# Optimization experiments

Measured on AMD Instinct MI355X. Metric: run time of the kernel, lower is better.

The kernel has to match this reference:

```python
import jax, jax.numpy as jnp
import numpy as np

B, N, C = 4, 4096, 1024
H, D = 16, 64
EPS = 1e-6


def setup_inputs() -> dict:
    key = jax.random.key(0)
    ks = jax.random.split(key, 7)
    x = jax.random.normal(ks[0], (B, N, C), dtype=jnp.float32)
    # True = PAD (PyTorch convention)
    src_key_padding_mask = jax.random.randint(ks[1], (B, N), 0, 2).astype(jnp.bool_)
    s = 1.0 / np.sqrt(C)
    W_qkv = jax.random.uniform(ks[2], (3 * C, C), jnp.float32, -s, s)
    b_qkv = jax.random.uniform(ks[3], (3 * C,), jnp.float32, -s, s)
    W_out = jax.random.uniform(ks[4], (C, C), jnp.float32, -s, s)
    b_out = jax.random.uniform(ks[5], (C,), jnp.float32, -s, s)
    return {"x": x, "W_qkv": W_qkv, "b_qkv": b_qkv, "W_out": W_out,
            "b_out": b_out, "src_key_padding_mask": src_key_padding_mask}


def _phi(t):
    # elu(t) + 1  (alpha=1)
    return jnp.where(t > 0, t + 1.0, jnp.exp(t))


def reference(x, W_qkv, b_qkv, W_out, b_out, src_key_padding_mask):
    # qkv projection: [B,N,3C] -> [3,B,H,N,D]
    qkv = (x @ W_qkv.T + b_qkv).reshape(B, N, 3, H, D).transpose(2, 0, 3, 1, 4)
    q, k, v = qkv[0], qkv[1], qkv[2]
    qf = _phi(q)
    kf = _phi(k)
    valid = (~src_key_padding_mask).astype(kf.dtype)[:, None, :, None]  # [B,1,N,1]
    kf = kf * valid
    v = v * valid
    # kv state: [B,H,D,D]; z: [B,H,D]
    kv = jnp.einsum('bhnd,bhne->bhde', kf, v)
    z = kf.sum(axis=2)
    y_num = jnp.einsum('bhnd,bhde->bhne', qf, kv)      # [B,H,N,D]
    y_den = jnp.einsum('bhnd,bhd->bhn', qf, z)          # [B,H,N]
    y_den = jnp.maximum(y_den, EPS)[..., None]
    y = (y_num / y_den).transpose(0, 2, 1, 3).reshape(B, N, C)
    return y @ W_out.T + b_out
```

## Files before the change

kernel.cpp:

```cpp
#include <hip/hip_runtime.h>
#include <math.h>

#define B_ 4
#define N_ 4096
#define C_ 1024
#define H_ 16
#define D_ 64
#define M_ (B_*N_)
#define GK 1024
#define NCH 8
#define CHROWS (N_/NCH)

typedef __attribute__((ext_vector_type(8))) _Float16 f16x8;
typedef __attribute__((ext_vector_type(4))) _Float16 f16x4;
typedef __attribute__((ext_vector_type(4))) float f32x4;

__device__ __forceinline__ float phi_f(float t) {
  return (t > 0.0f) ? (t + 1.0f) : __expf(t);
}

#define GLOAD(gp, lp) __builtin_amdgcn_global_load_lds( \
    (const __attribute__((address_space(1))) unsigned int*)(gp), \
    (__attribute__((address_space(3))) unsigned int*)(lp), 16, 0, 0)

#define BARM() asm volatile("s_barrier" ::: "memory")
#define WAITV6() asm volatile("s_waitcnt vmcnt(6)" ::: "memory")
#define WAITV4() asm volatile("s_waitcnt vmcnt(4)" ::: "memory")
#define WAITV0() asm volatile("s_waitcnt vmcnt(0)" ::: "memory")
#define PRIO1() __builtin_amdgcn_s_setprio(1)
#define PRIO0() __builtin_amdgcn_s_setprio(0)

__device__ __forceinline__ f32x4 mfma16h(f16x8 a, f16x8 b, f32x4 c) {
  return __builtin_amdgcn_mfma_f32_16x16x32_f16(a, b, c, 0, 0, 0);
}

__global__ __launch_bounds__(256) void prep_k(
    const float* __restrict__ x, _Float16* __restrict__ Xh,
    const float* __restrict__ Wq, _Float16* __restrict__ Wqh, _Float16* __restrict__ Wql,
    const float* __restrict__ Wo, _Float16* __restrict__ Woh, _Float16* __restrict__ Wol,
    const void* __restrict__ mask, float* __restrict__ valid) {
  const int b = blockIdx.x, tid = threadIdx.x;
  if (b < 16384) {
    int i = b * 256 + tid;
    float4 v = ((const float4*)x)[i];
    f16x4 h;
    h[0] = (_Float16)v.x; h[1] = (_Float16)v.y;
    h[2] = (_Float16)v.z; h[3] = (_Float16)v.w;
    ((f16x4*)Xh)[i] = h;
  } else if (b < 19456) {
    int i = (b - 16384) * 256 + tid;
    float4 v = ((const float4*)Wq)[i];
    float vs[4] = {v.x, v.y, v.z, v.w};
    f16x4 hv, lv;
#pragma unroll
    for (int q = 0; q < 4; ++q) {
      _Float16 hh = (_Float16)vs[q];
      lv[q] = (_Float16)(vs[q] - (float)hh);
      hv[q] = hh;
    }
    ((f16x4*)Wqh)[i] = hv;
    ((f16x4*)Wql)[i] = lv;
  } else if (b < 20480) {
    int i = (b - 19456) * 256 + tid;
    float4 v = ((const float4*)Wo)[i];
    float vs[4] = {v.x, v.y, v.z, v.w};
    f16x4 hv, lv;
#pragma unroll
    for (int q = 0; q < 4; ++q) {
      _Float16 hh = (_Float16)vs[q];
      lv[q] = (_Float16)(vs[q] - (float)hh);
      hv[q] = hh;
    }
    ((f16x4*)Woh)[i] = hv;
    ((f16x4*)Wol)[i] = lv;
  } else {
    __shared__ unsigned int sni, snf;
    if (tid == 0) { sni = 0u; snf = 0u; }
    __syncthreads();
    const unsigned int* mw = (const unsigned int*)mask;
    unsigned int ni = 0, nf = 0;
    for (int t = tid; t < 4096; t += 256) {
      unsigned int v = mw[t];
      ni |= (v > 1u) ? 1u : 0u;
      nf |= (v != 0u && v != 0x3F800000u) ? 1u : 0u;
    }
    if (ni) atomicOr(&sni, 1u);
    if (nf) atomicOr(&snf, 1u);
    __syncthreads();
    const int f = (!sni) ? 0 : ((!snf) ? 1 : 2);
    int i = (b - 20480) * 256 + tid;
    int m;
    if (f == 0)      m = ((const int*)mask)[i] != 0;
    else if (f == 1) m = ((const float*)mask)[i] != 0.0f;
    else             m = ((const unsigned char*)mask)[i] != 0;
    valid[i] = m ? 0.0f : 1.0f;
  }
}


#define TILE_BODY(PC, DO_STAGE, DO_PRE, WAITK, KS)                             \
  {                                                                            \
    const _Float16* bb = lds + (PC) * 24576;                                   \
    const _Float16* nb = lds + (((PC) + 1) % 3) * 24576;                       \
    _Float16* sq = lds + (((PC) + 2) % 3) * 24576;                             \
    const size_t ks = (KS);                                                    \
                                     \
    _Pragma("unroll") for (int j = 0; j < 4; ++j)                              \
      bl[j] = *(const f16x8*)&bb[16384 + (wj * 4 + j) * 512 + lane * 8];       \
    if (DO_STAGE) { GLOAD(A + gA0 + ks, sq + w * 512);                         \
                    GLOAD(A + gA1 + ks, sq + 4096 + w * 512); }                \
    BARM();                                                                    \
    PRIO1();                                                                   \
    _Pragma("unroll") for (int i = 0; i < 4; ++i)                              \
      _Pragma("unroll") for (int j = 0; j < 4; ++j)                            \
        acc[i][j] = mfma16h(a0[i], bh[j], acc[i][j]);                          \
    PRIO0();                                                                   \
        \
    _Pragma("unroll") for (int i = 0; i < 4; ++i)                              \
      a1[i] = *(const f16x8*)&bb[(wm * 8 + 4 + i) * 512 + lane * 8];           \
    if (DO_STAGE) { GLOAD(Bh + gB0 + ks, sq + 8192 + w * 512);                 \
                    GLOAD(Bh + gB1 + ks, sq + 12288 + w * 512); }              \
    if ((WAITK) == 1) { WAITV4(); } else if ((WAITK) == 2) { WAITV0(); }       \
    BARM();                                                                    \
    PRIO1();                                                                   \
    _Pragma("unroll") for (int i = 0; i < 4; ++i)                              \
      _Pragma("unroll") for (int j = 0; j < 4; ++j)                            \
        acc[i][j] = mfma16h(a0[i], bl[j], acc[i][j]);                          \
    PRIO0();                                                                   \
                                \
    if (DO_PRE) { _Pragma("unroll") for (int i = 0; i < 4; ++i)                \
      a0[i] = *(const f16x8*)&nb[(wm * 8 + i) * 512 + lane * 8]; }             \
    if (DO_STAGE) { GLOAD(Bl + gB0 + ks, sq + 16384 + w * 512);                \
                    GLOAD(Bl + gB1 + ks, sq + 20480 + w * 512); }              \
    BARM();                                                                    \
    PRIO1();                                                                   \
    _Pragma("unroll") for (int i = 0; i < 4; ++i)                              \
      _Pragma("unroll") for (int j = 0; j < 4; ++j)                            \
        acc[4 + i][j] = mfma16h(a1[i], bh[j], acc[4 + i][j]);                  \
    PRIO0();                                                                   \
                                          \
    if (DO_PRE) { _Pragma("unroll") for (int j = 0; j < 4; ++j)                \
      bh[j] = *(const f16x8*)&nb[8192 + (wj * 4 + j) * 512 + lane * 8]; }      \
    BARM();                                                                    \
    PRIO1();                                                                   \
    _Pragma("unroll") for (int i = 0; i < 4; ++i)                              \
      _Pragma("unroll") for (int j = 0; j < 4; ++j)                            \
        acc[4 + i][j] = mfma16h(a1[i], bl[j], acc[4 + i][j]);                  \
    PRIO0();                                                                   \
  }

template <int EPI>
__global__ __launch_bounds__(512, 2) void gemm256_k(
    const _Float16* __restrict__ A,
    const _Float16* __restrict__ Bh, const _Float16* __restrict__ Bl,
    const float* __restrict__ bias, const float* __restrict__ valid,
    float* __restrict__ qf, float* __restrict__ kf, float* __restrict__ vv,
    float* __restrict__ outp, int jb) {
  __shared__ _Float16 lds[73728];
  const int tid = threadIdx.x;
  const int lane = tid & 63, w = tid >> 6;
  const int lm = lane & 15, lq = lane >> 4;
  const int wm = w >> 2, wj = w & 3;

  const int nwg = gridDim.x;
  const int q8 = nwg >> 3;
  const int wid = (blockIdx.x & 7) * q8 + (blockIdx.x >> 3);
  const int j_blk = wid >> 6;
  const int m_blk = wid & 63;
  const int m0 = m_blk * 256;
  const int jg0 = jb + j_blk * 256;

  const size_t gA0 = (size_t)(m0 + w * 16 + lm) * GK + lq * 8;
  const size_t gA1 = gA0 + (size_t)128 * GK;
  const size_t gB0 = (size_t)(jg0 + w * 16 + lm) * GK + lq * 8;
  const size_t gB1 = gB0 + (size_t)128 * GK;

#pragma unroll
  for (int tt = 0; tt < 2; ++tt) {
    _Float16* sq = lds + tt * 24576;
    const size_t ks = (size_t)tt * 32;
    GLOAD(A + gA0 + ks, sq + w * 512);
    GLOAD(A + gA1 + ks, sq + 4096 + w * 512);
    GLOAD(Bh + gB0 + ks, sq + 8192 + w * 512);
    GLOAD(Bh + gB1 + ks, sq + 12288 + w * 512);
    GLOAD(Bl + gB0 + ks, sq + 16384 + w * 512);
    GLOAD(Bl + gB1 + ks, sq + 20480 + w * 512);
  }
  WAITV6();
  BARM();

  f32x4 acc[8][4] = {};
  f16x8 a0[4], a1[4], bh[4], bl[4];
#pragma unroll
  for (int i = 0; i < 4; ++i)
    a0[i] = *(const f16x8*)&lds[(wm * 8 + i) * 512 + lane * 8];
#pragma unroll
  for (int j = 0; j < 4; ++j)
    bh[j] = *(const f16x8*)&lds[8192 + (wj * 4 + j) * 512 + lane * 8];

  for (int it = 0; it < 10; ++it) {
    const int t0 = 3 * it;
    TILE_BODY(0, true, true, 1, (size_t)(t0 + 2) * 32)
    TILE_BODY(1, true, true, 1, (size_t)(t0 + 3) * 32)
    TILE_BODY(2, true, true, 1, (size_t)(t0 + 4) * 32)
  }
  TILE_BODY(0, false, true, 2, 0)
  TILE_BODY(1, false, false, 0, 0)

  if (EPI == 0) {
    const int ty = jg0 >> 10;
    float* dst = (ty == 0) ? qf : ((ty == 1) ? kf : vv);
    float vld[8][4];
#pragma unroll
    for (int i = 0; i < 8; ++i)
#pragma unroll
      for (int r = 0; r < 4; ++r)
        vld[i][r] = (ty == 0) ? 1.0f : valid[m0 + wm * 128 + i * 16 + lq * 4 + r];
#pragma unroll
    for (int jt = 0; jt < 4; ++jt) {
      int jcol = jg0 + wj * 64 + jt * 16 + lm;
      float bj = bias[jcol];
      int c = jcol & 1023, hd = c >> 6, d = c & 63;
#pragma unroll
      for (int i = 0; i < 8; ++i)
#pragma unroll
        for (int r = 0; r < 4; ++r) {
          int m = m0 + wm * 128 + i * 16 + lq * 4 + r;
          int b = m >> 12, n = m & 4095;
          float val = acc[i][jt][r] + bj;
          if (ty <= 1) val = phi_f(val);
          if (ty >= 1) val *= vld[i][r];
          dst[(((size_t)(b * H_ + hd) * N_ + n) << 6) + d] = val;
        }
    }
  } else {
#pragma unroll
    for (int jt = 0; jt < 4; ++jt) {
      int jcol = jg0 + wj * 64 + jt * 16 + lm;
      float bj = bias[jcol];
#pragma unroll
      for (int i = 0; i < 8; ++i)
#pragma unroll
        for (int r = 0; r < 4; ++r) {
          int m = m0 + wm * 128 + i * 16 + lq * 4 + r;
          outp[(size_t)m * C_ + jcol] = acc[i][jt][r] + bj;
        }
    }
  }
}

__global__ __launch_bounds__(256) void kv_partial_k(
    const float* __restrict__ kf, const float* __restrict__ vv,
    float* __restrict__ kvp, float* __restrict__ zp) {
  const int bh = blockIdx.x, ch = blockIdx.y;
  const float* kfr = kf + ((size_t)bh * N_ + ch * CHROWS) * 64;
  const float* vr  = vv + ((size_t)bh * N_ + ch * CHROWS) * 64;
  __shared__ float vs[16][64];
  const int tid = threadIdx.x;
  const int d4 = tid >> 4, e4 = tid & 15;
  const int srow = tid >> 4, scol = (tid & 15) * 4;
  float acc[4][4] = {};
  float zacc[4] = {};
  for (int nb = 0; nb < CHROWS; nb += 16) {
    float4 st = *(const float4*)&vr[(size_t)(nb + srow) * 64 + scol];
    __syncthreads();
    *(float4*)&vs[srow][scol] = st;
    float4 kq[16];
#pragma unroll
    for (int r = 0; r < 16; ++r)
      kq[r] = *(const float4*)&kfr[(size_t)(nb + r) * 64 + d4 * 4];
    __syncthreads();
#pragma unroll
    for (int r = 0; r < 16; ++r) {
      float4 vq = *(const float4*)&vs[r][e4 * 4];
      float kk[4] = {kq[r].x, kq[r].y, kq[r].z, kq[r].w};
      float vk[4] = {vq.x, vq.y, vq.z, vq.w};
#pragma unroll
      for (int di = 0; di < 4; ++di) {
        if (e4 == 0) zacc[di] += kk[di];
#pragma unroll
        for (int ei = 0; ei < 4; ++ei) acc[di][ei] += kk[di] * vk[ei];
      }
    }
  }
  size_t base = ((size_t)bh * NCH + ch) * 4096 + (size_t)d4 * 4 * 64 + e4 * 4;
#pragma unroll
  for (int di = 0; di < 4; ++di)
    *(float4*)&kvp[base + (size_t)di * 64] =
        make_float4(acc[di][0], acc[di][1], acc[di][2], acc[di][3]);
  if (e4 == 0)
    *(float4*)&zp[((size_t)bh * NCH + ch) * 64 + d4 * 4] =
        make_float4(zacc[0], zacc[1], zacc[2], zacc[3]);
}

__global__ __launch_bounds__(256) void kv_reduce_k(
    const float* __restrict__ kvp, const float* __restrict__ zp,
    float* __restrict__ kv, float* __restrict__ z) {
  const int bh = blockIdx.x, tid = threadIdx.x;
  for (int i = tid; i < 4096; i += 256) {
    float s = 0.f;
#pragma unroll
    for (int c = 0; c < NCH; ++c) s += kvp[((size_t)bh * NCH + c) * 4096 + i];
    kv[(size_t)bh * 4096 + i] = s;
  }
  if (tid < 64) {
    float s = 0.f;
#pragma unroll
    for (int c = 0; c < NCH; ++c) s += zp[((size_t)bh * NCH + c) * 64 + tid];
    z[bh * 64 + tid] = s;
  }
}

__global__ __launch_bounds__(256) void attn_apply_k(
    const float* __restrict__ qf, const float* __restrict__ kv,
    const float* __restrict__ z, _Float16* __restrict__ Y) {
  const int bh = blockIdx.x, nt = blockIdx.y;
  const int b = bh >> 4, hd = bh & 15;
  __shared__ float qs[128][65];
  __shared__ float kvs[64][68];
  __shared__ float zs[64];
  __shared__ float dens[128];
  const int tid = threadIdx.x;
  const float* qrow = qf + ((size_t)bh * N_ + nt * 128) * 64;
#pragma unroll
  for (int i = 0; i < 4; ++i) {
    int fl = tid + i * 256;
    int d = fl >> 4, cc = (fl & 15) * 4;
    float4 t4 = *(const float4*)&kv[(size_t)bh * 4096 + d * 64 + cc];
    kvs[d][cc] = t4.x; kvs[d][cc+1] = t4.y; kvs[d][cc+2] = t4.z; kvs[d][cc+3] = t4.w;
  }
  if (tid < 64) zs[tid] = z[bh * 64 + tid];
#pragma unroll
  for (int i = 0; i < 8; ++i) {
    int fl = tid + i * 256;
    int r = fl >> 4, cc = (fl & 15) * 4;
    float4 t4 = *(const float4*)&qrow[(size_t)r * 64 + cc];
    qs[r][cc] = t4.x; qs[r][cc+1] = t4.y; qs[r][cc+2] = t4.z; qs[r][cc+3] = t4.w;
  }
  __syncthreads();
  {
    int n = tid >> 1, half = tid & 1;
    float s = 0.f;
#pragma unroll
    for (int dd = 0; dd < 32; ++dd) {
      int d = half * 32 + dd;
      s += qs[n][d] * zs[d];
    }
    float other = __shfl_down(s, 1);
    if (half == 0) dens[n] = fmaxf(s + other, 1e-6f);
  }
  __syncthreads();
  const int ng = tid >> 3, eg = tid & 7;
  float acc[4][8] = {};
  for (int d = 0; d < 64; ++d) {
    float kvrow[8];
    *(float4*)&kvrow[0] = *(const float4*)&kvs[d][eg * 8];
    *(float4*)&kvrow[4] = *(const float4*)&kvs[d][eg * 8 + 4];
#pragma unroll
    for (int i = 0; i < 4; ++i) {
      float a = qs[ng * 4 + i][d];
#pragma unroll
      for (int j = 0; j < 8; ++j) acc[i][j] += a * kvrow[j];
    }
  }
#pragma unroll
  for (int i = 0; i < 4; ++i) {
    int nl = ng * 4 + i;
    int n = nt * 128 + nl;
    float inv = 1.0f / dens[nl];
    size_t off = ((size_t)b * N_ + n) * C_ + hd * 64 + eg * 8;
    f16x8 hv;
#pragma unroll
    for (int j = 0; j < 8; ++j) hv[j] = (_Float16)(acc[i][j] * inv);
    *(f16x8*)&Y[off] = hv;
  }
}

extern "C" void kernel_launch(void* const* d_in, const int* in_sizes, int n_in,
                              void* d_out, int out_size, void* d_ws, size_t ws_size,
                              hipStream_t stream) {
  const float* x      = (const float*)d_in[0];
  const float* W_qkv  = (const float*)d_in[1];
  const float* b_qkv  = (const float*)d_in[2];
  const float* W_out  = (const float*)d_in[3];
  const float* b_out  = (const float*)d_in[4];
  const void*  mask   = d_in[5];
  float* out = (float*)d_out;

  const size_t bhnd = (size_t)B_ * H_ * N_ * D_;
  float* ws = (float*)d_ws;
  float* buf1 = ws;
  float* buf2 = ws + bhnd;
  _Float16* Xh  = (_Float16*)(ws + 2 * bhnd);
  _Float16* Wqh = Xh + bhnd;
  _Float16* Wql = Wqh + (size_t)3072 * 1024;
  _Float16* Woh = Wql + (size_t)3072 * 1024;
  _Float16* Wol = Woh + (size_t)1024 * 1024;
  float* tail2 = (float*)(Wol + (size_t)1024 * 1024);
  float* kvp = tail2;
  float* zp  = kvp + (size_t)64 * NCH * 4096;
  float* kv  = zp + (size_t)64 * NCH * 64;
  float* z   = kv + (size_t)64 * 4096;
  float* valid = z + 64 * 64;

  _Float16* Y = (_Float16*)buf2;

  prep_k<<<20544, 256, 0, stream>>>(x, Xh, W_qkv, Wqh, Wql, W_out, Woh, Wol,
                                    mask, valid);
  gemm256_k<0><<<512, 512, 0, stream>>>(
      Xh, Wqh, Wql, b_qkv, valid, buf1, buf1, buf2, nullptr, 1024);
  kv_partial_k<<<dim3(B_ * H_, NCH), 256, 0, stream>>>(buf1, buf2, kvp, zp);
  kv_reduce_k<<<B_ * H_, 256, 0, stream>>>(kvp, zp, kv, z);
  gemm256_k<0><<<256, 512, 0, stream>>>(
      Xh, Wqh, Wql, b_qkv, valid, buf1, buf1, buf2, nullptr, 0);
  attn_apply_k<<<dim3(B_ * H_, N_ / 128), 256, 0, stream>>>(buf1, kv, z, Y);
  gemm256_k<1><<<256, 512, 0, stream>>>(
      Y, Woh, Wol, b_out, valid, nullptr, nullptr, nullptr, out, 0);
}
```

Before: 483.8 us.

## Fuse attention apply into Q-projection GEMM epilogue using MFMA split-fp16

Result: no change. 475.7 us (-1.7%).

```diff
diff --git a/kernel.cpp b/kernel.cpp
--- a/kernel.cpp
+++ b/kernel.cpp
@@ -27,6 +27,8 @@
 #define WAITV6() asm volatile("s_waitcnt vmcnt(6)" ::: "memory")
 #define WAITV4() asm volatile("s_waitcnt vmcnt(4)" ::: "memory")
 #define WAITV0() asm volatile("s_waitcnt vmcnt(0)" ::: "memory")
+#define WAITL0() asm volatile("s_waitcnt lgkmcnt(0)" ::: "memory")
+#define SCHEDB() __builtin_amdgcn_sched_barrier(0)
 #define PRIO1() __builtin_amdgcn_s_setprio(1)
 #define PRIO0() __builtin_amdgcn_s_setprio(0)
 
@@ -155,7 +157,9 @@
     const _Float16* __restrict__ Bh, const _Float16* __restrict__ Bl,
     const float* __restrict__ bias, const float* __restrict__ valid,
     float* __restrict__ qf, float* __restrict__ kf, float* __restrict__ vv,
-    float* __restrict__ outp, int jb) {
+    float* __restrict__ outp, int jb, int jshift,
+    const _Float16* __restrict__ kvt_h, const _Float16* __restrict__ kvt_l,
+    const float* __restrict__ zv, _Float16* __restrict__ Yo) {
   __shared__ _Float16 lds[73728];
   const int tid = threadIdx.x;
   const int lane = tid & 63, w = tid >> 6;
@@ -165,8 +169,8 @@
   const int nwg = gridDim.x;
   const int q8 = nwg >> 3;
   const int wid = (blockIdx.x & 7) * q8 + (blockIdx.x >> 3);
-  const int j_blk = wid >> 6;
-  const int m_blk = wid & 63;
+  const int j_blk = wid & ((1 << jshift) - 1);
+  const int m_blk = wid >> jshift;
   const int m0 = m_blk * 256;
   const int jg0 = jb + j_blk * 256;
 
@@ -233,7 +237,7 @@
           dst[(((size_t)(b * H_ + hd) * N_ + n) << 6) + d] = val;
         }
     }
-  } else {
+  } else if (EPI == 1) {
 #pragma unroll
     for (int jt = 0; jt < 4; ++jt) {
       int jcol = jg0 + wj * 64 + jt * 16 + lm;
@@ -245,6 +249,92 @@
           int m = m0 + wm * 128 + i * 16 + lq * 4 + r;
           outp[(size_t)m * C_ + jcol] = acc[i][jt][r] + bj;
         }
+    }
+  } else {
+    const int head = (jg0 >> 6) + wj;
+    const int bidx = m0 >> 12;
+    const int bh_idx = bidx * H_ + head;
+    const size_t kvbase = (size_t)bh_idx * 4096;
+    float breg[4], zreg[4];
+#pragma unroll
+    for (int jt = 0; jt < 4; ++jt) {
+      breg[jt] = bias[jg0 + wj * 64 + jt * 16 + lm];
+      zreg[jt] = zv[bh_idx * 64 + jt * 16 + lm];
+    }
+    float den[8][4];
+#pragma unroll
+    for (int i = 0; i < 8; ++i)
+#pragma unroll
+      for (int r = 0; r < 4; ++r) {
+        float p = 0.f;
+#pragma unroll
+        for (int jt = 0; jt < 4; ++jt) {
+          float v = phi_f(acc[i][jt][r] + breg[jt]);
+          acc[i][jt][r] = v;
+          p += v * zreg[jt];
+        }
+        p += __shfl_xor(p, 1); p += __shfl_xor(p, 2);
+        p += __shfl_xor(p, 4); p += __shfl_xor(p, 8);
+        den[i][r] = 1.0f / fmaxf(p, 1e-6f);
+      }
+    BARM();
+    char* sb = (char*)(lds) + w * 16384;
+#pragma unroll
+    for (int h = 0; h < 2; ++h) {
+#pragma unroll
+      for (int i2 = 0; i2 < 4; ++i2) {
+#pragma unroll
+        for (int jt = 0; jt < 4; ++jt)
+#pragma unroll
+          for (int r = 0; r < 4; ++r) {
+            int row = i2 * 16 + lq * 4 + r;
+            int d = jt * 16 + lm;
+            float v = acc[h * 4 + i2][jt][r];
+            _Float16 vh = (_Float16)v;
+            _Float16 vl = (_Float16)(v - (float)vh);
+            int bo = (row * 128 + d * 2) ^ ((row & 7) << 4);
+            *(_Float16*)(sb + bo) = vh;
+            *(_Float16*)(sb + 8192 + bo) = vl;
+          }
+      }
+      WAITL0(); SCHEDB();
+      f32x4 acc2[4][4] = {};
+#pragma unroll
+      for (int ks = 0; ks < 2; ++ks) {
+        f16x8 ah[4], al[4], bhf[4], blf[4];
+#pragma unroll
+        for (int f = 0; f < 4; ++f) {
+          int row = f * 16 + lm;
+          int bo = (row * 128 + ks * 64 + lq * 16) ^ ((row & 7) << 4);
+          ah[f] = *(const f16x8*)(sb + bo);
+          al[f] = *(const f16x8*)(sb + 8192 + bo);
+        }
+#pragma unroll
+        for (int et = 0; et < 4; ++et) {
+          size_t go = kvbase + (size_t)(et * 16 + lm) * 64 + ks * 32 + lq * 8;
+          bhf[et] = *(const f16x8*)&kvt_h[go];
+          blf[et] = *(const f16x8*)&kvt_l[go];
+        }
+#pragma unroll
+        for (int f = 0; f < 4; ++f)
+#pragma unroll
+          for (int et = 0; et < 4; ++et) {
+            acc2[f][et] = mfma16h(ah[f], bhf[et], acc2[f][et]);
+            acc2[f][et] = mfma16h(ah[f], blf[et], acc2[f][et]);
+            acc2[f][et] = mfma16h(al[f], bhf[et], acc2[f][et]);
+          }
+      }
+#pragma unroll
+      for (int f = 0; f < 4; ++f)
+#pragma unroll
+        for (int et = 0; et < 4; ++et)
+#pragma unroll
+          for (int r = 0; r < 4; ++r) {
+            int m = m0 + wm * 128 + h * 64 + f * 16 + lq * 4 + r;
+            float yv = acc2[f][et][r] * den[h * 4 + f][r];
+            Yo[(size_t)m * C_ + head * 64 + et * 16 + lm] = (_Float16)yv;
+          }
+      WAITL0(); SCHEDB();
     }
   }
 }
@@ -295,84 +385,23 @@
 
 __global__ __launch_bounds__(256) void kv_reduce_k(
     const float* __restrict__ kvp, const float* __restrict__ zp,
-    float* __restrict__ kv, float* __restrict__ z) {
+    _Float16* __restrict__ kvt_h, _Float16* __restrict__ kvt_l,
+    float* __restrict__ z) {
   const int bh = blockIdx.x, tid = threadIdx.x;
   for (int i = tid; i < 4096; i += 256) {
     float s = 0.f;
 #pragma unroll
     for (int c = 0; c < NCH; ++c) s += kvp[((size_t)bh * NCH + c) * 4096 + i];
-    kv[(size_t)bh * 4096 + i] = s;
+    int d = i >> 6, e = i & 63;
+    _Float16 sh = (_Float16)s;
+    kvt_h[(size_t)bh * 4096 + e * 64 + d] = sh;
+    kvt_l[(size_t)bh * 4096 + e * 64 + d] = (_Float16)(s - (float)sh);
   }
   if (tid < 64) {
     float s = 0.f;
 #pragma unroll
     for (int c = 0; c < NCH; ++c) s += zp[((size_t)bh * NCH + c) * 64 + tid];
     z[bh * 64 + tid] = s;
-  }
-}
-
-__global__ __launch_bounds__(256) void attn_apply_k(
-    const float* __restrict__ qf, const float* __restrict__ kv,
-    const float* __restrict__ z, _Float16* __restrict__ Y) {
-  const int bh = blockIdx.x, nt = blockIdx.y;
-  const int b = bh >> 4, hd = bh & 15;
-  __shared__ float qs[128][65];
-  __shared__ float kvs[64][68];
-  __shared__ float zs[64];
-  __shared__ float dens[128];
-  const int tid = threadIdx.x;
-  const float* qrow = qf + ((size_t)bh * N_ + nt * 128) * 64;
-#pragma unroll
-  for (int i = 0; i < 4; ++i) {
-    int fl = tid + i * 256;
-    int d = fl >> 4, cc = (fl & 15) * 4;
-    float4 t4 = *(const float4*)&kv[(size_t)bh * 4096 + d * 64 + cc];
-    kvs[d][cc] = t4.x; kvs[d][cc+1] = t4.y; kvs[d][cc+2] = t4.z; kvs[d][cc+3] = t4.w;
-  }
-  if (tid < 64) zs[tid] = z[bh * 64 + tid];
-#pragma unroll
-  for (int i = 0; i < 8; ++i) {
-    int fl = tid + i * 256;
-    int r = fl >> 4, cc = (fl & 15) * 4;
-    float4 t4 = *(const float4*)&qrow[(size_t)r * 64 + cc];
-    qs[r][cc] = t4.x; qs[r][cc+1] = t4.y; qs[r][cc+2] = t4.z; qs[r][cc+3] = t4.w;
-  }
-  __syncthreads();
-  {
-    int n = tid >> 1, half = tid & 1;
-    float s = 0.f;
-#pragma unroll
-    for (int dd = 0; dd < 32; ++dd) {
-      int d = half * 32 + dd;
-      s += qs[n][d] * zs[d];
-    }
-    float other = __shfl_down(s, 1);
-    if (half == 0) dens[n] = fmaxf(s + other, 1e-6f);
-  }
-  __syncthreads();
-  const int ng = tid >> 3, eg = tid & 7;
-  float acc[4][8] = {};
-  for (int d = 0; d < 64; ++d) {
-    float kvrow[8];
-    *(float4*)&kvrow[0] = *(const float4*)&kvs[d][eg * 8];
-    *(float4*)&kvrow[4] = *(const float4*)&kvs[d][eg * 8 + 4];
-#pragma unroll
-    for (int i = 0; i < 4; ++i) {
-      float a = qs[ng * 4 + i][d];
-#pragma unroll
-      for (int j = 0; j < 8; ++j) acc[i][j] += a * kvrow[j];
-    }
-  }
-#pragma unroll
-  for (int i = 0; i < 4; ++i) {
-    int nl = ng * 4 + i;
-    int n = nt * 128 + nl;
-    float inv = 1.0f / dens[nl];
-    size_t off = ((size_t)b * N_ + n) * C_ + hd * 64 + eg * 8;
-    f16x8 hv;
-#pragma unroll
-    for (int j = 0; j < 8; ++j) hv[j] = (_Float16)(acc[i][j] * inv);
-    *(f16x8*)&Y[off] = hv;
   }
 }
 
@@ -399,21 +428,24 @@
   float* tail2 = (float*)(Wol + (size_t)1024 * 1024);
   float* kvp = tail2;
   float* zp  = kvp + (size_t)64 * NCH * 4096;
-  float* kv  = zp + (size_t)64 * NCH * 64;
-  float* z   = kv + (size_t)64 * 4096;
+  float* z   = zp + (size_t)64 * NCH * 64;
   float* valid = z + 64 * 64;
+  _Float16* kvt_h = (_Float16*)(valid + M_);
+  _Float16* kvt_l = kvt_h + (size_t)64 * 4096;
 
   _Float16* Y = (_Float16*)buf2;
 
   prep_k<<<20544, 256, 0, stream>>>(x, Xh, W_qkv, Wqh, Wql, W_out, Woh, Wol,
                                     mask, valid);
   gemm256_k<0><<<512, 512, 0, stream>>>(
-      Xh, Wqh, Wql, b_qkv, valid, buf1, buf1, buf2, nullptr, 1024);
+      Xh, Wqh, Wql, b_qkv, valid, buf1, buf1, buf2, nullptr, 1024, 3,
+      nullptr, nullptr, nullptr, nullptr);
   kv_partial_k<<<dim3(B_ * H_, NCH), 256, 0, stream>>>(buf1, buf2, kvp, zp);
-  kv_reduce_k<<<B_ * H_, 256, 0, stream>>>(kvp, zp, kv, z);
-  gemm256_k<0><<<256, 512, 0, stream>>>(
-      Xh, Wqh, Wql, b_qkv, valid, buf1, buf1, buf2, nullptr, 0);
-  attn_apply_k<<<dim3(B_ * H_, N_ / 128), 256, 0, stream>>>(buf1, kv, z, Y);
+  kv_reduce_k<<<B_ * H_, 256, 0, stream>>>(kvp, zp, kvt_h, kvt_l, z);
+  gemm256_k<2><<<256, 512, 0, stream>>>(
+      Xh, Wqh, Wql, b_qkv, valid, nullptr, nullptr, nullptr, nullptr, 0, 2,
+      kvt_h, kvt_l, z, Y);
   gemm256_k<1><<<256, 512, 0, stream>>>(
-      Y, Woh, Wol, b_out, valid, nullptr, nullptr, nullptr, out, 0);
-}
+      Y, Woh, Wol, b_out, valid, nullptr, nullptr, nullptr, out, 0, 2,
+      nullptr, nullptr, nullptr, nullptr);
+}
```
